# Optimization experiments

Hardware: AMD Instinct MI355X
Metric: run time of the kernel (lower is better)

The kernel has to match this reference:

```python
import jax, jax.numpy as jnp
import numpy as np


def setup_inputs() -> dict:
    key = jax.random.key(0)
    ks = jax.random.split(key, 7)
    B, H, W = 32, 28, 28
    C3, C4 = 1024, 2048
    C = C3 + C4            # 3072
    L1 = 9                 # num_landmarks + 1
    A, NC = 312, 200
    return {
        "l3": jax.random.normal(ks[0], (B, C3, H, W), jnp.float32),
        "l4": jax.random.normal(ks[1], (B, C4, H // 2, W // 2), jnp.float32),
        "conv_w": jax.random.normal(ks[2], (L1, C), jnp.float32) * 0.02,
        "modulation": jnp.ones((1, C, L1), jnp.float32),
        "attr_w": jax.random.normal(ks[3], (A, C), jnp.float32) * 0.02,
        "attr_b": jnp.zeros((A,), jnp.float32),
        "class_w": jax.random.normal(ks[4], (NC, A), jnp.float32) * 0.02,
    }


def reference(l3, l4, conv_w, modulation, attr_w, attr_b, class_w):
    b, c3, h, w = l3.shape
    # F.interpolate(l4, (h, w), mode='bilinear', align_corners=False)
    l4_up = jax.image.resize(l4, (b, l4.shape[1], h, w), method="bilinear")
    x = jnp.concatenate([l4_up, l3], axis=1)            # (b, 3072, h, w)

    # 1x1 conv: ab[b,l,h,w] = sum_c w[l,c] * x[b,c,h,w]
    ab = jnp.einsum("lc,bchw->blhw", conv_w, x)
    b_sq = jnp.sum(x * x, axis=1, keepdims=True)        # (b,1,h,w)
    a_sq = jnp.sum(conv_w, axis=1)[None, :, None, None]  # (1,L+1,1,1)  (matches torch: weight.sum(1), NOT squared)
    maps = jax.nn.softmax(-(b_sq - 2.0 * ab + a_sq), axis=1)  # Softmax2d = softmax over channels

    # (maps[:,None] * x[:,:,None]).mean((-1,-2))  ->  batched GEMM over spatial dim
    all_features = jnp.einsum("blhw,bchw->bcl", maps, x) / (h * w)  # (b, c, L+1)

    mod = all_features * modulation                     # dropout is identity at eval
    # permute(0,2,1)[:, :-1, :].mean(1) == mean over landmark dim excluding background
    mean_features = jnp.mean(mod[:, :, :-1], axis=2)    # (b, c)

    attr_scores = mean_features @ attr_w.T + attr_b      # (b, 312)
    class_scores = attr_scores @ class_w.T               # (b, 200)
    return attr_scores, class_scores, maps, all_features
```

## Files before the change

### kernel.cpp

```cpp
#include <hip/hip_runtime.h>
#include <math.h>

#define B_    32
#define C3_   1024
#define C4_   2048
#define C_    3072
#define P_    784
#define Q_    196
#define L_    9
#define NG_   25088
#define A_    312
#define NC_   200

#define ATTR_OFF  0
#define CLASS_OFF 9984
#define MAPS_OFF  16384
#define AF_OFF    242176

#define ASQ_OFF   0
#define MF_OFF    16
#define PART3_OFF 98320
#define PAF_OFF   98320
#define Y4P_OFF   (PART3_OFF + 16 * 9 * NG_)
#define Y_OFF     (Y4P_OFF + 32 * 32 * 9 * Q_)
#define MP_OFF    (Y_OFF + 32 * 9 * Q_)

typedef __attribute__((ext_vector_type(8))) short bf16x8;
typedef __attribute__((ext_vector_type(4))) float f32x4;

__device__ __forceinline__ short f2bf(float f) {
    union { float f; unsigned u; } v; v.f = f;
    unsigned r = v.u + 0x7FFFu + ((v.u >> 16) & 1u);
    return (short)(r >> 16);
}

__global__ __launch_bounds__(256) void kA(
        const float* __restrict__ l3, const float* __restrict__ l4,
        const float* __restrict__ conv_w,
        float* __restrict__ part3, float* __restrict__ y4p,
        float* __restrict__ asq) {
    int bid = blockIdx.x;
    int t = threadIdx.x;
    if (bid < 392) {
        int tid = bid * 256 + t;
        int slab = tid / 6272;
        int rem = tid % 6272;
        int b = rem / 196, chunk = rem % 196;
        int px = chunk * 4;
        int c0 = slab * 64;
        const float* xp = l3 + ((size_t)b * C3_ + c0) * P_ + px;
        float ab[9][4];
#pragma unroll
        for (int l = 0; l < 9; ++l)
#pragma unroll
            for (int j = 0; j < 4; ++j) ab[l][j] = 0.f;
        for (int c = 0; c < 64; c += 8) {
            float4 v[8];
#pragma unroll
            for (int k = 0; k < 8; ++k)
                v[k] = *(const float4*)(xp + (size_t)(c + k) * P_);
#pragma unroll
            for (int l = 0; l < 9; ++l) {
                const float4 w0 = *(const float4*)(conv_w + l * C_ + C4_ + c0 + c);
                const float4 w1 = *(const float4*)(conv_w + l * C_ + C4_ + c0 + c + 4);
                const float wv[8] = {w0.x, w0.y, w0.z, w0.w, w1.x, w1.y, w1.z, w1.w};
#pragma unroll
                for (int k = 0; k < 8; ++k) {
                    ab[l][0] = fmaf(wv[k], v[k].x, ab[l][0]);
                    ab[l][1] = fmaf(wv[k], v[k].y, ab[l][1]);
                    ab[l][2] = fmaf(wv[k], v[k].z, ab[l][2]);
                    ab[l][3] = fmaf(wv[k], v[k].w, ab[l][3]);
                }
            }
        }
#pragma unroll
        for (int l = 0; l < 9; ++l)
            *(float4*)(part3 + (size_t)(slab * 9 + l) * NG_ + b * P_ + px) =
                make_float4(ab[l][0], ab[l][1], ab[l][2], ab[l][3]);
    } else if (bid < 588) {
        int tid = (bid - 392) * 256 + t;
        int grp = tid / 1568;
        int rem = tid % 1568;
        int b = rem / 49, chunk = rem % 49;
        int q = chunk * 4;
        int c0 = grp * 64;
        const float* xp = l4 + ((size_t)b * C4_ + c0) * Q_ + q;
        float ac[9][4];
#pragma unroll
        for (int l = 0; l < 9; ++l)
#pragma unroll
            for (int j = 0; j < 4; ++j) ac[l][j] = 0.f;
        for (int c = 0; c < 64; c += 8) {
            float4 v[8];
#pragma unroll
            for (int k = 0; k < 8; ++k)
                v[k] = *(const float4*)(xp + (size_t)(c + k) * Q_);
#pragma unroll
            for (int l = 0; l < 9; ++l) {
                const float4 w0 = *(const float4*)(conv_w + l * C_ + c0 + c);
                const float4 w1 = *(const float4*)(conv_w + l * C_ + c0 + c + 4);
                const float wv[8] = {w0.x, w0.y, w0.z, w0.w, w1.x, w1.y, w1.z, w1.w};
#pragma unroll
                for (int k = 0; k < 8; ++k) {
                    ac[l][0] = fmaf(wv[k], v[k].x, ac[l][0]);
                    ac[l][1] = fmaf(wv[k], v[k].y, ac[l][1]);
                    ac[l][2] = fmaf(wv[k], v[k].z, ac[l][2]);
                    ac[l][3] = fmaf(wv[k], v[k].w, ac[l][3]);
                }
            }
        }
#pragma unroll
        for (int l = 0; l < 9; ++l)
            *(float4*)(y4p + (size_t)((b * 32 + grp) * 9 + l) * Q_ + q) =
                make_float4(ac[l][0], ac[l][1], ac[l][2], ac[l][3]);
    } else {
        __shared__ float red[256];
        for (int l = 0; l < L_; ++l) {
            float s = 0.f;
            for (int c = t; c < C_; c += 256) s += conv_w[l * C_ + c];
            red[t] = s; __syncthreads();
            for (int o = 128; o > 0; o >>= 1) {
                if (t < o) red[t] += red[t + o];
                __syncthreads();
            }
            if (t == 0) asq[l] = red[0];
            __syncthreads();
        }
    }
}

__global__ __launch_bounds__(256) void kB(const float* __restrict__ y4p,
                                          float* __restrict__ Y) {
    int tid = blockIdx.x * 256 + threadIdx.x;
    if (tid >= 32 * 9 * Q_) return;
    int b = tid / (9 * Q_);
    int r = tid % (9 * Q_);
    float s = 0.f;
#pragma unroll
    for (int grp = 0; grp < 32; ++grp)
        s += y4p[(size_t)(b * 32 + grp) * (9 * Q_) + r];
    Y[(size_t)b * (9 * Q_) + r] = s;
}

__global__ __launch_bounds__(256) void kC(const float* __restrict__ part3,
                                          const float* __restrict__ Y,
                                          const float* __restrict__ asq,
                                          float* __restrict__ out_maps) {
    int g = blockIdx.x * 256 + threadIdx.x;
    int b = g / P_, p = g % P_;
    int yy = p / 28, xx = p % 28;
    float sy = 0.5f * yy - 0.25f, sx = 0.5f * xx - 0.25f;
    float fyf = floorf(sy), fxf = floorf(sx);
    float fy = sy - fyf, fx = sx - fxf;
    int ya = max(0, (int)fyf), yb = min(13, (int)fyf + 1);
    int xa = max(0, (int)fxf), xb = min(13, (int)fxf + 1);
    int o00 = ya * 14 + xa, o01 = ya * 14 + xb;
    int o10 = yb * 14 + xa, o11 = yb * 14 + xb;
    float w00 = (1.f - fy) * (1.f - fx), w01 = (1.f - fy) * fx;
    float w10 = fy * (1.f - fx),         w11 = fy * fx;
    const float* Yb = Y + (size_t)b * (9 * Q_);
    float v[9];
#pragma unroll
    for (int l = 0; l < 9; ++l) {
        const float* Yl = Yb + l * Q_;
        float ab4 = w00 * Yl[o00] + w01 * Yl[o01] + w10 * Yl[o10] + w11 * Yl[o11];
        float ab3 = 0.f;
#pragma unroll
        for (int sl = 0; sl < 16; ++sl)
            ab3 += part3[(size_t)(sl * 9 + l) * NG_ + g];
        v[l] = 2.f * (ab4 + ab3) - asq[l];
    }
    float m = v[0];
#pragma unroll
    for (int l = 1; l < 9; ++l) m = fmaxf(m, v[l]);
    float sum = 0.f;
#pragma unroll
    for (int l = 0; l < 9; ++l) { v[l] = expf(v[l] - m); sum += v[l]; }
    float inv = 1.f / sum;
#pragma unroll
    for (int l = 0; l < 9; ++l)
        out_maps[(size_t)b * (L_ * P_) + l * P_ + p] = v[l] * inv;
}

__device__ __forceinline__ int adj_taps(int q, int* ys, float* wy) {
    if (q == 0)  { ys[0] = 0;  wy[0] = 1.00f; ys[1] = 1;  wy[1] = 0.75f;
                   ys[2] = 2;  wy[2] = 0.25f; return 3; }
    if (q == 13) { ys[0] = 25; wy[0] = 0.25f; ys[1] = 26; wy[1] = 0.75f;
                   ys[2] = 27; wy[2] = 1.00f; return 3; }
    ys[0] = 2 * q - 1; wy[0] = 0.25f;
    ys[1] = 2 * q;     wy[1] = 0.75f;
    ys[2] = 2 * q + 1; wy[2] = 0.75f;
    ys[3] = 2 * q + 2; wy[3] = 0.25f;
    return 4;
}

__global__ __launch_bounds__(256) void kD(const float* __restrict__ maps,
                                          float* __restrict__ Mp) {
    int tid = blockIdx.x * 256 + threadIdx.x;
    if (tid >= 32 * 9 * Q_) return;
    int b = tid / (9 * Q_);
    int r = tid % (9 * Q_);
    int l = r / Q_, q = r % Q_;
    int qy = q / 14, qx = q % 14;
    int ys[4], xs[4]; float wy[4], wx[4];
    int ny = adj_taps(qy, ys, wy);
    int nx = adj_taps(qx, xs, wx);
    const float* mrow = maps + (size_t)b * (L_ * P_) + l * P_;
    float s = 0.f;
    for (int i = 0; i < ny; ++i) {
        float rs = 0.f;
        for (int j = 0; j < nx; ++j)
            rs = fmaf(wx[j], mrow[ys[i] * 28 + xs[j]], rs);
        s = fmaf(wy[i], rs, s);
    }
    Mp[(size_t)b * (9 * Q_) + r] = s;
}

#define SA 232
__global__ __launch_bounds__(256) void kE(
        const float* __restrict__ l3, const float* __restrict__ l4,
        const float* __restrict__ maps, const float* __restrict__ Mp,
        float* __restrict__ out_af, float* __restrict__ paf) {
    __shared__ short As[64 * SA];
    __shared__ short Bs[16 * SA];
    int bid = blockIdx.x;
    int t = threadIdx.x;
    int wave = t >> 6, lane = t & 63;
    int row16 = lane & 15, quad = lane >> 4;

    const float* xsrc; size_t xstride;
    const float* bsrc; size_t bstride;
    int b, c0, h;
    bool isl4 = (bid < 1024);
    if (isl4) {
        b = bid >> 5;
        c0 = (bid & 31) * 64;
        h = 0;
        xsrc = l4 + ((size_t)b * C4_ + c0) * Q_;
        xstride = Q_;
        bsrc = Mp + (size_t)b * (9 * Q_);
        bstride = Q_;
    } else {
        int idx = bid - 1024;
        b = idx >> 6;
        c0 = ((idx >> 2) & 15) * 64;
        h = idx & 3;
        xsrc = l3 + ((size_t)b * C3_ + c0) * P_ + h * Q_;
        xstride = P_;
        bsrc = maps + (size_t)b * (L_ * P_) + h * Q_;
        bstride = P_;
    }

    for (int i = t; i < 64 * 49; i += 256) {
        int r = i / 49, j = (i % 49) * 4;
        float4 v = *(const float4*)(xsrc + (size_t)r * xstride + j);
        ushort4 o;
        o.x = (unsigned short)f2bf(v.x); o.y = (unsigned short)f2bf(v.y);
        o.z = (unsigned short)f2bf(v.z); o.w = (unsigned short)f2bf(v.w);
        *(ushort4*)(As + r * SA + j) = o;
    }
    for (int i = t; i < 64 * 9; i += 256) {
        int r = i / 9, j = 196 + (i % 9) * 4;
        *(ushort4*)(As + r * SA + j) = make_ushort4(0, 0, 0, 0);
    }
    for (int i = t; i < 16 * 58; i += 256) {
        int r = i / 58, j = (i % 58) * 4;
        ushort4 o = make_ushort4(0, 0, 0, 0);
        if (r < 9 && j < 196) {
            float4 v = *(const float4*)(bsrc + (size_t)r * bstride + j);
            o.x = (unsigned short)f2bf(v.x); o.y = (unsigned short)f2bf(v.y);
            o.z = (unsigned short)f2bf(v.z); o.w = (unsigned short)f2bf(v.w);
        }
        *(ushort4*)(Bs + r * SA + j) = o;
    }
    __syncthreads();

    const short* arow = As + (wave * 16 + row16) * SA;
    const short* brow = Bs + row16 * SA;
    f32x4 acc = {0.f, 0.f, 0.f, 0.f};
#pragma unroll
    for (int k0 = 0; k0 < 224; k0 += 32) {
        bf16x8 a = *(const bf16x8*)(arow + k0 + quad * 8);
        bf16x8 bv = *(const bf16x8*)(brow + k0 + quad * 8);
        acc = __builtin_amdgcn_mfma_f32_16x16x32_bf16(a, bv, acc, 0, 0, 0);
    }
    int l = row16;
    if (l < 9) {
        int c = c0 + wave * 16 + quad * 4;
        if (isl4) {
            size_t base = ((size_t)b * C_ + c) * 9 + l;
#pragma unroll
            for (int r = 0; r < 4; ++r)
                out_af[base + (size_t)r * 9] = acc[r] * (1.f / 784.f);
        } else {
            size_t base = ((size_t)(h * B_ + b) * C3_ + c) * 9 + l;
#pragma unroll
            for (int r = 0; r < 4; ++r)
                paf[base + (size_t)r * 9] = acc[r];
        }
    }
}

__global__ __launch_bounds__(256) void kMF(const float* __restrict__ paf,
                                           const float* __restrict__ mod,
                                           float* __restrict__ out_af,
                                           float* __restrict__ mf) {
    int i = blockIdx.x * 256 + threadIdx.x;
    if (i >= B_ * C_) return;
    int b = i / C_, c = i % C_;
    float af[9];
    if (c < C4_) {
#pragma unroll
        for (int l = 0; l < 9; ++l) af[l] = out_af[(size_t)i * 9 + l];
    } else {
        int c3 = c - C4_;
#pragma unroll
        for (int l = 0; l < 9; ++l) {
            float s = 0.f;
#pragma unroll
            for (int hh = 0; hh < 4; ++hh)
                s += paf[((size_t)(hh * B_ + b) * C3_ + c3) * 9 + l];
            af[l] = s * (1.f / 784.f);
            out_af[(size_t)i * 9 + l] = af[l];
        }
    }
    const float* m = mod + (size_t)c * 9;
    float s = 0.f;
#pragma unroll
    for (int l = 0; l < 8; ++l) s = fmaf(af[l], m[l], s);
    mf[i] = s * 0.125f;
}

__global__ __launch_bounds__(256) void kF(
        const float* __restrict__ mf, const float* __restrict__ attr_w,
        const float* __restrict__ attr_b, float* __restrict__ out_attr) {
    int idx = blockIdx.x * 4 + (threadIdx.x >> 6);
    int lane = threadIdx.x & 63;
    int b = idx / A_, a = idx % A_;
    const float4* wr = (const float4*)(attr_w + (size_t)a * C_);
    const float4* mr = (const float4*)(mf + (size_t)b * C_);
    float acc = 0.f;
    for (int j = lane; j < C_ / 4; j += 64) {
        float4 w = wr[j], m = mr[j];
        acc += w.x * m.x + w.y * m.y + w.z * m.z + w.w * m.w;
    }
    acc += __shfl_xor(acc, 1);  acc += __shfl_xor(acc, 2);
    acc += __shfl_xor(acc, 4);  acc += __shfl_xor(acc, 8);
    acc += __shfl_xor(acc, 16); acc += __shfl_xor(acc, 32);
    if (lane == 0) out_attr[idx] = acc + attr_b[a];
}

__global__ __launch_bounds__(256) void kG(
        const float* __restrict__ attr, const float* __restrict__ class_w,
        float* __restrict__ out_class) {
    int idx = blockIdx.x * 4 + (threadIdx.x >> 6);
    int lane = threadIdx.x & 63;
    int b = idx / NC_, n = idx % NC_;
    float acc = 0.f;
    for (int a = lane; a < A_; a += 64)
        acc += attr[b * A_ + a] * class_w[n * A_ + a];
    acc += __shfl_xor(acc, 1);  acc += __shfl_xor(acc, 2);
    acc += __shfl_xor(acc, 4);  acc += __shfl_xor(acc, 8);
    acc += __shfl_xor(acc, 16); acc += __shfl_xor(acc, 32);
    if (lane == 0) out_class[idx] = acc;
}

extern "C" void kernel_launch(void* const* d_in, const int* in_sizes, int n_in,
                              void* d_out, int out_size, void* d_ws, size_t ws_size,
                              hipStream_t stream) {
    (void)in_sizes; (void)n_in; (void)out_size; (void)ws_size;
    const float* l3         = (const float*)d_in[0];
    const float* l4         = (const float*)d_in[1];
    const float* conv_w     = (const float*)d_in[2];
    const float* modulation = (const float*)d_in[3];
    const float* attr_w     = (const float*)d_in[4];
    const float* attr_b     = (const float*)d_in[5];
    const float* class_w    = (const float*)d_in[6];
    float* out = (float*)d_out;
    float* ws  = (float*)d_ws;
    float* asq   = ws + ASQ_OFF;
    float* mf    = ws + MF_OFF;
    float* part3 = ws + PART3_OFF;
    float* paf   = ws + PAF_OFF;
    float* y4p   = ws + Y4P_OFF;
    float* Y     = ws + Y_OFF;
    float* Mp    = ws + MP_OFF;

    kA<<<589, 256, 0, stream>>>(l3, l4, conv_w, part3, y4p, asq);
    kB<<<221, 256, 0, stream>>>(y4p, Y);
    kC<<<98, 256, 0, stream>>>(part3, Y, asq, out + MAPS_OFF);
    kD<<<221, 256, 0, stream>>>(out + MAPS_OFF, Mp);
    kE<<<3072, 256, 0, stream>>>(l3, l4, out + MAPS_OFF, Mp, out + AF_OFF, paf);
    kMF<<<384, 256, 0, stream>>>(paf, modulation, out + AF_OFF, mf);
    kF<<<(B_ * A_) / 4, 256, 0, stream>>>(mf, attr_w, attr_b, out + ATTR_OFF);
    kG<<<(B_ * NC_) / 4, 256, 0, stream>>>(out + ATTR_OFF, class_w,
                                           out + CLASS_OFF);
}
```

Baseline: 317.7 us.

## Double-buffer channel loads in conv kernel and split softmax logits across landmarks

Unifies the l3/l4 1x1-conv paths in kA, aligns block boundaries to slabs, adds register double-buffering of the channel loads, and sets a min-occupancy launch bound. The conv_w row-sum is moved from kA into an extra kB block. The old kC is split in two: kC1 computes logits with one thread per landmark-pixel, giving 9x more parallelism for the 16-slab reduction, and kC2 then runs the softmax. The split costs an extra launch and a logits round trip through the workspace, which reuses the y4p region after kB has consumed it.

```diff
diff --git a/kernel.cpp b/kernel.cpp
--- a/kernel.cpp
+++ b/kernel.cpp
@@ -22,6 +22,7 @@
 #define PART3_OFF 98320
 #define PAF_OFF   98320
 #define Y4P_OFF   (PART3_OFF + 16 * 9 * NG_)
+#define LOGITS_OFF Y4P_OFF
 #define Y_OFF     (Y4P_OFF + 32 * 32 * 9 * Q_)
 #define MP_OFF    (Y_OFF + 32 * 9 * Q_)
 
@@ -34,87 +35,85 @@
     return (short)(r >> 16);
 }
 
-__global__ __launch_bounds__(256) void kA(
+__global__ __launch_bounds__(256, 4) void kA(
         const float* __restrict__ l3, const float* __restrict__ l4,
         const float* __restrict__ conv_w,
-        float* __restrict__ part3, float* __restrict__ y4p,
-        float* __restrict__ asq) {
+        float* __restrict__ part3, float* __restrict__ y4p) {
     int bid = blockIdx.x;
     int t = threadIdx.x;
-    if (bid < 392) {
-        int tid = bid * 256 + t;
-        int slab = tid / 6272;
-        int rem = tid % 6272;
-        int b = rem / 196, chunk = rem % 196;
-        int px = chunk * 4;
-        int c0 = slab * 64;
-        const float* xp = l3 + ((size_t)b * C3_ + c0) * P_ + px;
-        float ab[9][4];
-#pragma unroll
-        for (int l = 0; l < 9; ++l)
-#pragma unroll
-            for (int j = 0; j < 4; ++j) ab[l][j] = 0.f;
-        for (int c = 0; c < 64; c += 8) {
-            float4 v[8];
+
+    const float* xp;
+    float* outp;
+    int xpitch, opitch, cbase_w;
+    if (bid < 400) {
+        int slab = bid / 25, rb = bid % 25;
+        int tid2 = rb * 256 + t;
+        if (tid2 >= 6272) return;
+        int b = tid2 / 196, px = (tid2 % 196) * 4;
+        xp = l3 + ((size_t)b * C3_ + slab * 64) * P_ + px;
+        xpitch = P_;
+        cbase_w = C4_ + slab * 64;
+        outp = part3 + (size_t)(slab * 9) * NG_ + b * P_ + px;
+        opitch = NG_;
+    } else {
+        int idx = bid - 400;
+        int grp = idx / 7, rb = idx % 7;
+        int tid2 = rb * 256 + t;
+        if (tid2 >= 1568) return;
+        int b = tid2 / 49, q = (tid2 % 49) * 4;
+        xp = l4 + ((size_t)b * C4_ + grp * 64) * Q_ + q;
+        xpitch = Q_;
+        cbase_w = grp * 64;
+        outp = y4p + ((size_t)(b * 32 + grp) * 9) * Q_ + q;
+        opitch = Q_;
+    }
+
+    float acc[9][4];
+#pragma unroll
+    for (int l = 0; l < 9; ++l)
+#pragma unroll
+        for (int j = 0; j < 4; ++j) acc[l][j] = 0.f;
+
+    float4 v[2][8];
+#pragma unroll
+    for (int k = 0; k < 8; ++k)
+        v[0][k] = *(const float4*)(xp + (size_t)k * xpitch);
+
+#pragma unroll
+    for (int c = 0; c < 64; c += 8) {
+        int cur = (c >> 3) & 1, nxt = cur ^ 1;
+        if (c < 56) {
 #pragma unroll
             for (int k = 0; k < 8; ++k)
-                v[k] = *(const float4*)(xp + (size_t)(c + k) * P_);
-#pragma unroll
-            for (int l = 0; l < 9; ++l) {
-                const float4 w0 = *(const float4*)(conv_w + l * C_ + C4_ + c0 + c);
-                const float4 w1 = *(const float4*)(conv_w + l * C_ + C4_ + c0 + c + 4);
-                const float wv[8] = {w0.x, w0.y, w0.z, w0.w, w1.x, w1.y, w1.z, w1.w};
-#pragma unroll
-                for (int k = 0; k < 8; ++k) {
-                    ab[l][0] = fmaf(wv[k], v[k].x, ab[l][0]);
-                    ab[l][1] = fmaf(wv[k], v[k].y, ab[l][1]);
-                    ab[l][2] = fmaf(wv[k], v[k].z, ab[l][2]);
-                    ab[l][3] = fmaf(wv[k], v[k].w, ab[l][3]);
-                }
+                v[nxt][k] = *(const float4*)(xp + (size_t)(c + 8 + k) * xpitch);
+        }
+#pragma unroll
+        for (int l = 0; l < 9; ++l) {
+            const float4 w0 = *(const float4*)(conv_w + l * C_ + cbase_w + c);
+            const float4 w1 = *(const float4*)(conv_w + l * C_ + cbase_w + c + 4);
+            const float wv[8] = {w0.x, w0.y, w0.z, w0.w, w1.x, w1.y, w1.z, w1.w};
+#pragma unroll
+            for (int k = 0; k < 8; ++k) {
+                acc[l][0] = fmaf(wv[k], v[cur][k].x, acc[l][0]);
+                acc[l][1] = fmaf(wv[k], v[cur][k].y, acc[l][1]);
+                acc[l][2] = fmaf(wv[k], v[cur][k].z, acc[l][2]);
+                acc[l][3] = fmaf(wv[k], v[cur][k].w, acc[l][3]);
             }
         }
-#pragma unroll
-        for (int l = 0; l < 9; ++l)
-            *(float4*)(part3 + (size_t)(slab * 9 + l) * NG_ + b * P_ + px) =
-                make_float4(ab[l][0], ab[l][1], ab[l][2], ab[l][3]);
-    } else if (bid < 588) {
-        int tid = (bid - 392) * 256 + t;
-        int grp = tid / 1568;
-        int rem = tid % 1568;
-        int b = rem / 49, chunk = rem % 49;
-        int q = chunk * 4;
-        int c0 = grp * 64;
-        const float* xp = l4 + ((size_t)b * C4_ + c0) * Q_ + q;
-        float ac[9][4];
-#pragma unroll
-        for (int l = 0; l < 9; ++l)
-#pragma unroll
-            for (int j = 0; j < 4; ++j) ac[l][j] = 0.f;
-        for (int c = 0; c < 64; c += 8) {
-            float4 v[8];
-#pragma unroll
-            for (int k = 0; k < 8; ++k)
-                v[k] = *(const float4*)(xp + (size_t)(c + k) * Q_);
-#pragma unroll
-            for (int l = 0; l < 9; ++l) {
-                const float4 w0 = *(const float4*)(conv_w + l * C_ + c0 + c);
-                const float4 w1 = *(const float4*)(conv_w + l * C_ + c0 + c + 4);
-                const float wv[8] = {w0.x, w0.y, w0.z, w0.w, w1.x, w1.y, w1.z, w1.w};
-#pragma unroll
-                for (int k = 0; k < 8; ++k) {
-                    ac[l][0] = fmaf(wv[k], v[k].x, ac[l][0]);
-                    ac[l][1] = fmaf(wv[k], v[k].y, ac[l][1]);
-                    ac[l][2] = fmaf(wv[k], v[k].z, ac[l][2]);
-                    ac[l][3] = fmaf(wv[k], v[k].w, ac[l][3]);
-                }
-            }
-        }
-#pragma unroll
-        for (int l = 0; l < 9; ++l)
-            *(float4*)(y4p + (size_t)((b * 32 + grp) * 9 + l) * Q_ + q) =
-                make_float4(ac[l][0], ac[l][1], ac[l][2], ac[l][3]);
-    } else {
+    }
+#pragma unroll
+    for (int l = 0; l < 9; ++l)
+        *(float4*)(outp + (size_t)l * opitch) =
+            make_float4(acc[l][0], acc[l][1], acc[l][2], acc[l][3]);
+}
+
+__global__ __launch_bounds__(256) void kB(const float* __restrict__ y4p,
+                                          const float* __restrict__ conv_w,
+                                          float* __restrict__ Y,
+                                          float* __restrict__ asq) {
+    if (blockIdx.x == 221) {
         __shared__ float red[256];
+        int t = threadIdx.x;
         for (int l = 0; l < L_; ++l) {
             float s = 0.f;
             for (int c = t; c < C_; c += 256) s += conv_w[l * C_ + c];
@@ -126,11 +125,8 @@
             if (t == 0) asq[l] = red[0];
             __syncthreads();
         }
-    }
-}
-
-__global__ __launch_bounds__(256) void kB(const float* __restrict__ y4p,
-                                          float* __restrict__ Y) {
+        return;
+    }
     int tid = blockIdx.x * 256 + threadIdx.x;
     if (tid >= 32 * 9 * Q_) return;
     int b = tid / (9 * Q_);
@@ -142,11 +138,12 @@
     Y[(size_t)b * (9 * Q_) + r] = s;
 }
 
-__global__ __launch_bounds__(256) void kC(const float* __restrict__ part3,
-                                          const float* __restrict__ Y,
-                                          const float* __restrict__ asq,
-                                          float* __restrict__ out_maps) {
-    int g = blockIdx.x * 256 + threadIdx.x;
+__global__ __launch_bounds__(256) void kC1(const float* __restrict__ part3,
+                                           const float* __restrict__ Y,
+                                           const float* __restrict__ asq,
+                                           float* __restrict__ logits) {
+    int idx = blockIdx.x * 256 + threadIdx.x;
+    int l = idx / NG_, g = idx % NG_;
     int b = g / P_, p = g % P_;
     int yy = p / 28, xx = p % 28;
     float sy = 0.5f * yy - 0.25f, sx = 0.5f * xx - 0.25f;
@@ -154,22 +151,25 @@
     float fy = sy - fyf, fx = sx - fxf;
     int ya = max(0, (int)fyf), yb = min(13, (int)fyf + 1);
     int xa = max(0, (int)fxf), xb = min(13, (int)fxf + 1);
-    int o00 = ya * 14 + xa, o01 = ya * 14 + xb;
-    int o10 = yb * 14 + xa, o11 = yb * 14 + xb;
     float w00 = (1.f - fy) * (1.f - fx), w01 = (1.f - fy) * fx;
     float w10 = fy * (1.f - fx),         w11 = fy * fx;
-    const float* Yb = Y + (size_t)b * (9 * Q_);
+    const float* Yl = Y + ((size_t)b * 9 + l) * Q_;
+    float ab4 = w00 * Yl[ya * 14 + xa] + w01 * Yl[ya * 14 + xb]
+              + w10 * Yl[yb * 14 + xa] + w11 * Yl[yb * 14 + xb];
+    float ab3 = 0.f;
+#pragma unroll
+    for (int sl = 0; sl < 16; ++sl)
+        ab3 += part3[(size_t)(sl * 9 + l) * NG_ + g];
+    logits[idx] = 2.f * (ab4 + ab3) - asq[l];
+}
+
+__global__ __launch_bounds__(256) void kC2(const float* __restrict__ logits,
+                                           float* __restrict__ out_maps) {
+    int g = blockIdx.x * 256 + threadIdx.x;
+    int b = g / P_, p = g % P_;
     float v[9];
 #pragma unroll
-    for (int l = 0; l < 9; ++l) {
-        const float* Yl = Yb + l * Q_;
-        float ab4 = w00 * Yl[o00] + w01 * Yl[o01] + w10 * Yl[o10] + w11 * Yl[o11];
-        float ab3 = 0.f;
-#pragma unroll
-        for (int sl = 0; sl < 16; ++sl)
-            ab3 += part3[(size_t)(sl * 9 + l) * NG_ + g];
-        v[l] = 2.f * (ab4 + ab3) - asq[l];
-    }
+    for (int l = 0; l < 9; ++l) v[l] = logits[(size_t)l * NG_ + g];
     float m = v[0];
 #pragma unroll
     for (int l = 1; l < 9; ++l) m = fmaxf(m, v[l]);
@@ -378,17 +378,19 @@
     const float* class_w    = (const float*)d_in[6];
     float* out = (float*)d_out;
     float* ws  = (float*)d_ws;
-    float* asq   = ws + ASQ_OFF;
-    float* mf    = ws + MF_OFF;
-    float* part3 = ws + PART3_OFF;
-    float* paf   = ws + PAF_OFF;
-    float* y4p   = ws + Y4P_OFF;
-    float* Y     = ws + Y_OFF;
-    float* Mp    = ws + MP_OFF;
-
-    kA<<<589, 256, 0, stream>>>(l3, l4, conv_w, part3, y4p, asq);
-    kB<<<221, 256, 0, stream>>>(y4p, Y);
-    kC<<<98, 256, 0, stream>>>(part3, Y, asq, out + MAPS_OFF);
+    float* asq    = ws + ASQ_OFF;
+    float* mf     = ws + MF_OFF;
+    float* part3  = ws + PART3_OFF;
+    float* paf    = ws + PAF_OFF;
+    float* y4p    = ws + Y4P_OFF;
+    float* logits = ws + LOGITS_OFF;
+    float* Y      = ws + Y_OFF;
+    float* Mp     = ws + MP_OFF;
+
+    kA<<<624, 256, 0, stream>>>(l3, l4, conv_w, part3, y4p);
+    kB<<<222, 256, 0, stream>>>(y4p, conv_w, Y, asq);
+    kC1<<<882, 256, 0, stream>>>(part3, Y, asq, logits);
+    kC2<<<98, 256, 0, stream>>>(logits, out + MAPS_OFF);
     kD<<<221, 256, 0, stream>>>(out + MAPS_OFF, Mp);
     kE<<<3072, 256, 0, stream>>>(l3, l4, out + MAPS_OFF, Mp, out + AF_OFF, paf);
     kMF<<<384, 256, 0, stream>>>(paf, modulation, out + AF_OFF, mf);
```

After: 307.9 us. -3.1%, faster.
